# Kernel optimization log

Measured on AMD Instinct MI355X. Metric: run time of the kernel, lower is better.

Reference implementation:

```python
import jax, jax.numpy as jnp
import numpy as np

N = 100000      # num_nodes
E = 500000      # num_edges
D = 128         # memory_dim (also per-head out channels of TransformerConv)
EF = 16         # edge_feat_dim
H = 2           # heads
OUT = 64        # classifier out_channels


def setup_inputs() -> dict:
    key = jax.random.key(0)
    ks = jax.random.split(key, 24)
    g = lambda k, shape, s=0.05: (jax.random.normal(k, shape, jnp.float32) * s)
    inp = {
        "edge_index": jax.random.randint(ks[0], (2, E), 0, N, dtype=jnp.int64),
        "edge_attr": jax.random.normal(ks[1], (E, EF), jnp.float32),
        "edge_time": jax.random.uniform(ks[2], (E,), jnp.float32),
        # memory buffer (non-trainable in torch); randn so gathers are non-trivial
        "memory": g(ks[3], (N, D), 0.1),
        # MessageModule MLP: Linear(2D+EF -> D), ReLU, Linear(D -> D)
        "w1": g(ks[4], (2 * D + EF, D)), "b1": g(ks[5], (D,)),
        "w2": g(ks[6], (D, D)), "b2": g(ks[7], (D,)),
        # GRUCell(D, D): torch layout [3D, D] with gate order r,z,n
        "gru_wih": g(ks[8], (3 * D, D)), "gru_whh": g(ks[9], (3 * D, D)),
        "gru_bih": g(ks[10], (3 * D,)), "gru_bhh": g(ks[11], (3 * D,)),
        # TransformerConv(D, D, heads=H): lin_query/key/value: D -> H*D, lin_skip: D -> H*D
        "wq": g(ks[12], (D, H * D)), "bq": g(ks[13], (H * D,)),
        "wk": g(ks[14], (D, H * D)), "bk": g(ks[15], (H * D,)),
        "wv": g(ks[16], (D, H * D)), "bv": g(ks[17], (H * D,)),
        "wskip": g(ks[18], (D, H * D)), "bskip": g(ks[19], (H * D,)),
        # classifier: H*D -> OUT
        "wc": g(ks[20], (H * D, OUT)), "bc": g(ks[21], (OUT,)),
    }
    return inp


def reference(edge_index, edge_attr, edge_time, memory, w1, b1, w2, b2,
              gru_wih, gru_whh, gru_bih, gru_bhh,
              wq, bq, wk, bk, wv, bv, wskip, bskip, wc, bc):
    n_nodes = memory.shape[0]
    src, dst = edge_index[0], edge_index[1]
    # memory is a requires_grad=False parameter in torch
    mem = jax.lax.stop_gradient(memory)

    # ---- message computation (gather + MLP) ----
    src_mem = mem[src]                      # [E, D]
    dst_mem = mem[dst]                      # [E, D]
    msg_in = jnp.concatenate([src_mem, dst_mem, edge_attr], axis=-1)
    messages = jax.nn.relu(msg_in @ w1 + b1) @ w2 + b2   # [E, D]

    # ---- GRUCell memory update (torch gate order: r, z, n) ----
    gi = messages @ gru_wih.T + gru_bih     # [E, 3D]
    gh = dst_mem @ gru_whh.T + gru_bhh      # [E, 3D]
    i_r, i_z, i_n = jnp.split(gi, 3, axis=-1)
    h_r, h_z, h_n = jnp.split(gh, 3, axis=-1)
    r = jax.nn.sigmoid(i_r + h_r)
    z = jax.nn.sigmoid(i_z + h_z)
    n = jnp.tanh(i_n + r * h_n)
    new_mem = (1.0 - z) * n + z * dst_mem   # [E, D]
    # detached scatter write (memory.data[node_ids] = updated_mem.data)
    node_mem = mem.at[dst].set(jax.lax.stop_gradient(new_mem))  # [N, D]

    # ---- TransformerConv(D, D, heads=H), concat=True, root_weight=True ----
    q = (node_mem @ wq + bq).reshape(n_nodes, H, D)
    k = (node_mem @ wk + bk).reshape(n_nodes, H, D)
    v = (node_mem @ wv + bv).reshape(n_nodes, H, D)
    # per-edge attention logits, aggregated at destination node
    logits = jnp.sum(q[dst] * k[src], axis=-1) / jnp.sqrt(jnp.float32(D))  # [E, H]
    m = jax.ops.segment_max(logits, dst, num_segments=n_nodes)             # [N, H]
    ex = jnp.exp(logits - m[dst])
    s = jax.ops.segment_sum(ex, dst, num_segments=n_nodes)                 # [N, H]
    alpha = ex / (s[dst] + 1e-16)                                          # [E, H]
    agg = jax.ops.segment_sum(v[src] * alpha[..., None], dst,
                              num_segments=n_nodes)                        # [N, H, D]
    conv_out = agg.reshape(n_nodes, H * D) + node_mem @ wskip + bskip

    # ---- classifier ----
    return conv_out @ wc + bc               # [N, OUT]
```

## Files before the change

kernel.cpp:

```cpp
#include <hip/hip_runtime.h>
#include <hip/hip_bf16.h>

#define DD 128
#define EFD 16
#define HDIM 256
#define OUTD 64
#define AW 296

#define P_W1T 0
#define P_W2T 36864
#define P_WIH 53248
#define P_WHH 102400
#define P_QKV 151552
#define P_WSK 249856
#define P_WCT 282624
#define P_TOT 299008

using bf16 = __hip_bfloat16;
typedef __attribute__((ext_vector_type(8))) short fab;
typedef __attribute__((ext_vector_type(4))) float f4;

__device__ __forceinline__ float b2f(bf16 x){ return __bfloat162float(x); }
__device__ __forceinline__ bf16  f2b(float x){ return __float2bfloat16(x); }
__device__ __forceinline__ unsigned short us(bf16 x){ return *(unsigned short*)&x; }
__device__ __forceinline__ float rawbf(unsigned int u16){
  return __uint_as_float(u16 << 16);
}
__device__ __forceinline__ unsigned pk2(float a, float b){
  return (unsigned)us(f2b(a)) | ((unsigned)us(f2b(b)) << 16);
}
__device__ __forceinline__ float gw(const void* p, size_t i, int f32){
  return f32 ? ((const float*)p)[i] : b2f(((const bf16*)p)[i]);
}
__device__ __forceinline__ uint2 ld4bf(const void* base, size_t off, int f32){
  if(f32){
    float4 v = *(const float4*)((const float*)base + off);
    uint2 r;
    r.x = pk2(v.x, v.y);
    r.y = pk2(v.z, v.w);
    return r;
  }
  return *(const uint2*)((const bf16*)base + off);
}
__device__ __forceinline__ int geti(const int* ei, int is64, long long idx){
  return is64 ? ei[2*idx] : ei[(size_t)idx];
}
__device__ __forceinline__ int clampi(int x, int hi){
  return x < 0 ? 0 : (x >= hi ? hi-1 : x);
}

__global__ void k_detect(const int* __restrict__ ei,
                         const unsigned short* __restrict__ mem16,
                         int* __restrict__ flags){
  __shared__ int s64, sf32;
  int t = threadIdx.x;
  if(t == 0){ s64 = 1; sf32 = 0; }
  __syncthreads();
  if(ei[2*t + 1] != 0) atomicAnd(&s64, 0);
  int cnt = 0;
  for(int i = t; i < 4096; i += 256){
    unsigned short h = mem16[2*i];
    if((h & 0x7f80u) >= 0x4000u) cnt++;
  }
  atomicAdd(&sf32, cnt);
  __syncthreads();
  if(t == 0){ flags[0] = s64; flags[1] = (sf32 > 8) ? 1 : 0; }
}

__global__ void k_init(int* winner, int* cntrp, int N){
  int i = blockIdx.x*blockDim.x + threadIdx.x;
  if(i < N) winner[i] = -1;
  if(i <= N) cntrp[i] = 0;
}

__global__ void k_winner(const int* __restrict__ ei, const int* __restrict__ flags,
                         int* winner, int* cntrp, int E, int N){
  int e = blockIdx.x*blockDim.x + threadIdx.x;
  if(e >= E) return;
  int d = clampi(geti(ei, flags[0], (long long)E + e), N);
  atomicMax(&winner[d], e);
  atomicAdd(&cntrp[d], 1);
}

__global__ void k_scanA(const int* __restrict__ cnt, int* __restrict__ bsum, int N, int P){
  __shared__ int sd[256];
  int b = blockIdx.x, t = threadIdx.x;
  int base = (b*256 + t)*P;
  int s = 0;
  for(int p=0;p<P;p++){ int i = base+p; if(i<N) s += cnt[i]; }
  sd[t] = s; __syncthreads();
  for(int off=128; off>0; off>>=1){
    if(t<off) sd[t] += sd[t+off];
    __syncthreads();
  }
  if(t==0) bsum[b] = sd[0];
}

__global__ void k_scanB(const int* __restrict__ bsum, int* __restrict__ boff,
                        int* __restrict__ rowptr, int N, int E){
  __shared__ int sd[256];
  int t = threadIdx.x;
  int v = bsum[t];
  sd[t] = v; __syncthreads();
  for(int off=1; off<256; off<<=1){
    int u = (t>=off) ? sd[t-off] : 0;
    __syncthreads();
    sd[t] += u;
    __syncthreads();
  }
  boff[t] = sd[t] - v;
  if(t==0) rowptr[N] = E;
}

__global__ void k_scanC(int* __restrict__ cntrp, const int* __restrict__ boff,
                        int* __restrict__ head, int N, int P){
  __shared__ int sd[256];
  int b = blockIdx.x, t = threadIdx.x;
  int base = (b*256 + t)*P;
  int loc[8];
  int s = 0;
  for(int p=0;p<P;p++){ int i=base+p; int cc=(i<N)?cntrp[i]:0; loc[p]=s; s+=cc; }
  sd[t]=s; __syncthreads();
  for(int off=1; off<256; off<<=1){
    int u=(t>=off)?sd[t-off]:0;
    __syncthreads(); sd[t]+=u; __syncthreads();
  }
  int start = boff[b] + sd[t] - s;
  for(int p=0;p<P;p++){
    int i=base+p;
    if(i<N){ int r = start + loc[p]; cntrp[i]=r; head[i]=r; }
  }
}

__global__ void k_scatter(const int* __restrict__ ei, const int* __restrict__ flags,
                          int* __restrict__ head, int* __restrict__ esrc, int E, int N){
  int e = blockIdx.x*256 + threadIdx.x;
  if(e >= E) return;
  int is64 = flags[0];
  int src = clampi(geti(ei, is64, e), N);
  int dst = clampi(geti(ei, is64, (long long)E + e), N);
  int slot = atomicAdd(&head[dst], 1);
  esrc[slot] = src;
}

__global__ void k_pack(const void* w1, const void* w2, const void* wih, const void* whh,
                       const void* wq, const void* wk, const void* wv,
                       const void* wsk, const void* wc,
                       const int* __restrict__ flags, bf16* __restrict__ pk){
  int i = blockIdx.x*256 + threadIdx.x;
  if(i >= P_TOT) return;
  int f = flags[1];
  float v;
  if(i < P_W2T){ int j = i/288, c = i%288; v = (c < 272) ? gw(w1,(size_t)c*DD + j, f) : 0.f; }
  else if(i < P_WIH){ int r = i - P_W2T; int j = r>>7, c = r&127; v = gw(w2,(size_t)c*DD + j, f); }
  else if(i < P_WHH){ v = gw(wih, i - P_WIH, f); }
  else if(i < P_QKV){ v = gw(whh, i - P_WHH, f); }
  else if(i < P_WSK){
    int r = i - P_QKV; int jj = r>>7, c = r&127;
    int tb = jj>>8, j = jj&255;
    const void* w = (tb==0) ? wq : ((tb==1) ? wk : wv);
    v = gw(w, (size_t)c*HDIM + j, f);
  }
  else if(i < P_WCT){ int r = i - P_WSK; int j = r>>7, c = r&127; v = gw(wsk,(size_t)c*HDIM + j, f); }
  else { int r = i - P_WCT; int o = r>>8, j = r&255; v = gw(wc,(size_t)j*OUTD + o, f); }
  pk[i] = f2b(v);
}

__global__ __launch_bounds__(512) void k_msggru_qkv(
    const int* __restrict__ ei, const void* __restrict__ eattr,
    const void* __restrict__ mem, const bf16* __restrict__ pk,
    const void* b1, const void* b2, const void* bih, const void* bhh,
    const void* bq, const void* bk, const void* bv,
    const int* __restrict__ winner, const int* __restrict__ flags,
    bf16* __restrict__ node_mem, bf16* __restrict__ qt, bf16* __restrict__ kv, int N){
  const bf16* pw1T = pk + P_W1T;
  const bf16* pw2T = pk + P_W2T;
  const bf16* pwih = pk + P_WIH;
  const bf16* pwhh = pk + P_WHH;
  __shared__ bf16 Abuf[128][AW];
  __shared__ int swin[128], ssrc[128];
  int t = threadIdx.x;
  int n0 = blockIdx.x*128;
  int f = flags[1], is64 = flags[0];
  if(t < 128){
    int n = n0 + t;
    int w = (n < N) ? winner[n] : -1;
    swin[t] = w;
    ssrc[t] = (w >= 0) ? clampi(geti(ei, is64, w), N) : 0;
  }
  __syncthreads();
  const uint2 z2 = {0u, 0u};
  for(int idx=t; idx<128*32; idx+=512){
    int i = idx>>5, c4 = (idx&31)*4;
    int w = swin[i], n = n0+i;
    uint2 sv = (w>=0) ? ld4bf(mem, (size_t)ssrc[i]*DD + c4, f) : z2;
    uint2 dv = (n<N)  ? ld4bf(mem, (size_t)n*DD + c4, f)      : z2;
    *(uint2*)&Abuf[i][c4]    = sv;
    *(uint2*)&Abuf[i][DD+c4] = dv;
  }
  for(int idx=t; idx<128*4; idx+=512){
    int i = idx>>2, c4 = (idx&3)*4;
    uint2 v = (swin[i]>=0) ? ld4bf(eattr, (size_t)swin[i]*EFD + c4, f) : z2;
    *(uint2*)&Abuf[i][256+c4] = v;
  }
  for(int idx=t; idx<128*6; idx+=512){
    int i = idx/6, c4 = 272 + (idx%6)*4;
    *(uint2*)&Abuf[i][c4] = z2;
  }
  __syncthreads();

  int lane  = t & 63;
  int wid   = t >> 6;
  int col16 = lane & 15;
  int quad  = lane >> 4;
  int q8    = quad*8;
  int ch    = wid*16 + quad*4;

  {
    uint2 hres[8];
    const bf16* wrow = pw1T + (size_t)(wid*16 + col16)*288 + q8;
    fab w[9];
    #pragma unroll
    for(int kc=0;kc<9;kc++) w[kc] = *(const fab*)(wrow + kc*32);
    float bb0 = gw(b1, ch,   f), bb1 = gw(b1, ch+1, f);
    float bb2 = gw(b1, ch+2, f), bb3 = gw(b1, ch+3, f);
    #pragma unroll
    for(int mt=0; mt<8; mt++){
      f4 acc = (f4){0.f,0.f,0.f,0.f};
      #pragma unroll
      for(int kc=0;kc<9;kc++){
        fab an = *(const fab*)&Abuf[mt*16+col16][kc*32+q8];
        acc = __builtin_amdgcn_mfma_f32_16x16x32_bf16(w[kc], an, acc, 0,0,0);
      }
      uint2 hv;
      hv.x = pk2(fmaxf(acc[0]+bb0,0.f), fmaxf(acc[1]+bb1,0.f));
      hv.y = pk2(fmaxf(acc[2]+bb2,0.f), fmaxf(acc[3]+bb3,0.f));
      hres[mt] = hv;
    }
    __syncthreads();
    #pragma unroll
    for(int mt=0; mt<8; mt++)
      *(uint2*)&Abuf[mt*16+col16][ch] = hres[mt];
    __syncthreads();
  }

  {
    uint2 mres[8];
    const bf16* wrow = pw2T + (size_t)(wid*16 + col16)*128 + q8;
    fab w[4];
    #pragma unroll
    for(int kc=0;kc<4;kc++) w[kc] = *(const fab*)(wrow + kc*32);
    float bb0 = gw(b2, ch,   f), bb1 = gw(b2, ch+1, f);
    float bb2 = gw(b2, ch+2, f), bb3 = gw(b2, ch+3, f);
    #pragma unroll
    for(int mt=0; mt<8; mt++){
      f4 acc = (f4){0.f,0.f,0.f,0.f};
      #pragma unroll
      for(int kc=0;kc<4;kc++){
        fab an = *(const fab*)&Abuf[mt*16+col16][kc*32+q8];
        acc = __builtin_amdgcn_mfma_f32_16x16x32_bf16(w[kc], an, acc, 0,0,0);
      }
      uint2 hv;
      hv.x = pk2(acc[0]+bb0, acc[1]+bb1);
      hv.y = pk2(acc[2]+bb2, acc[3]+bb3);
      mres[mt] = hv;
    }
    __syncthreads();
    #pragma unroll
    for(int mt=0; mt<8; mt++)
      *(uint2*)&Abuf[mt*16+col16][ch] = mres[mt];
    __syncthreads();
  }

  {
    uint2 ovals[8];
    size_t row = (size_t)(wid*16 + col16)*128;
    const bf16* wi = pwih + row + q8;
    const bf16* wh = pwhh + row + q8;
    float bR0 = gw(bih,ch,f)+gw(bhh,ch,f),     bR1 = gw(bih,ch+1,f)+gw(bhh,ch+1,f);
    float bR2 = gw(bih,ch+2,f)+gw(bhh,ch+2,f), bR3 = gw(bih,ch+3,f)+gw(bhh,ch+3,f);
    float bZ0 = gw(bih,128+ch,f)+gw(bhh,128+ch,f), bZ1 = gw(bih,129+ch,f)+gw(bhh,129+ch,f);
    float bZ2 = gw(bih,130+ch,f)+gw(bhh,130+ch,f), bZ3 = gw(bih,131+ch,f)+gw(bhh,131+ch,f);
    float bNi0 = gw(bih,256+ch,f), bNi1 = gw(bih,257+ch,f);
    float bNi2 = gw(bih,258+ch,f), bNi3 = gw(bih,259+ch,f);
    float bNh0 = gw(bhh,256+ch,f), bNh1 = gw(bhh,257+ch,f);
    float bNh2 = gw(bhh,258+ch,f), bNh3 = gw(bhh,259+ch,f);
    #pragma unroll
    for(int mt=0; mt<8; mt++){
      int arow = mt*16 + col16;
      f4 ri=(f4){0,0,0,0}, zi=(f4){0,0,0,0}, ni=(f4){0,0,0,0};
      #pragma unroll
      for(int kc=0;kc<4;kc++){
        int kb = kc*32;
        fab am = *(const fab*)&Abuf[arow][kb+q8];
        ri = __builtin_amdgcn_mfma_f32_16x16x32_bf16(*(const fab*)(wi+kb),       am, ri, 0,0,0);
        zi = __builtin_amdgcn_mfma_f32_16x16x32_bf16(*(const fab*)(wi+16384+kb), am, zi, 0,0,0);
        ni = __builtin_amdgcn_mfma_f32_16x16x32_bf16(*(const fab*)(wi+32768+kb), am, ni, 0,0,0);
      }
      f4 rh=(f4){0,0,0,0}, zh=(f4){0,0,0,0}, nh=(f4){0,0,0,0};
      #pragma unroll
      for(int kc=0;kc<4;kc++){
        int kb = kc*32;
        fab ad = *(const fab*)&Abuf[arow][DD+kb+q8];
        rh = __builtin_amdgcn_mfma_f32_16x16x32_bf16(*(const fab*)(wh+kb),       ad, rh, 0,0,0);
        zh = __builtin_amdgcn_mfma_f32_16x16x32_bf16(*(const fab*)(wh+16384+kb), ad, zh, 0,0,0);
        nh = __builtin_amdgcn_mfma_f32_16x16x32_bf16(*(const fab*)(wh+32768+kb), ad, nh, 0,0,0);
      }
      bool upd = (swin[arow] >= 0);
      uint2 hraw = *(const uint2*)&Abuf[arow][DD+ch];
      float hp0 = rawbf(hraw.x & 0xffffu), hp1 = rawbf(hraw.x >> 16);
      float hp2 = rawbf(hraw.y & 0xffffu), hp3 = rawbf(hraw.y >> 16);
      float o0, o1, o2, o3;
      if(upd){
        float rr0 = 1.f/(1.f+__expf(-(ri[0]+rh[0]+bR0)));
        float rr1 = 1.f/(1.f+__expf(-(ri[1]+rh[1]+bR1)));
        float rr2 = 1.f/(1.f+__expf(-(ri[2]+rh[2]+bR2)));
        float rr3 = 1.f/(1.f+__expf(-(ri[3]+rh[3]+bR3)));
        float zz0 = 1.f/(1.f+__expf(-(zi[0]+zh[0]+bZ0)));
        float zz1 = 1.f/(1.f+__expf(-(zi[1]+zh[1]+bZ1)));
        float zz2 = 1.f/(1.f+__expf(-(zi[2]+zh[2]+bZ2)));
        float zz3 = 1.f/(1.f+__expf(-(zi[3]+zh[3]+bZ3)));
        float nn0 = tanhf(ni[0]+bNi0 + rr0*(nh[0]+bNh0));
        float nn1 = tanhf(ni[1]+bNi1 + rr1*(nh[1]+bNh1));
        float nn2 = tanhf(ni[2]+bNi2 + rr2*(nh[2]+bNh2));
        float nn3 = tanhf(ni[3]+bNi3 + rr3*(nh[3]+bNh3));
        o0 = (1.f-zz0)*nn0 + zz0*hp0;
        o1 = (1.f-zz1)*nn1 + zz1*hp1;
        o2 = (1.f-zz2)*nn2 + zz2*hp2;
        o3 = (1.f-zz3)*nn3 + zz3*hp3;
      } else { o0 = hp0; o1 = hp1; o2 = hp2; o3 = hp3; }
      uint2 ov;
      ov.x = pk2(o0, o1);
      ov.y = pk2(o2, o3);
      ovals[mt] = ov;
      int n = n0 + arow;
      if(n < N) *(uint2*)&node_mem[(size_t)n*DD + ch] = ov;
    }
    __syncthreads();
    #pragma unroll
    for(int mt=0; mt<8; mt++)
      *(uint2*)&Abuf[mt*16+col16][ch] = ovals[mt];
    __syncthreads();
  }

  {
    const bf16* pq = pk + P_QKV;
    #pragma unroll 2
    for(int i=0;i<6;i++){
      int nt = wid*6 + i;
      const bf16* wrow = pq + (size_t)(nt*16 + col16)*128 + q8;
      fab w[4];
      #pragma unroll
      for(int kc=0;kc<4;kc++) w[kc] = *(const fab*)(wrow + kc*32);
      int dch = nt*16 + quad*4;
      int tb = dch >> 8, j = dch & 255;
      const void* bp = (tb==0) ? bq : ((tb==1) ? bk : bv);
      float bb0 = gw(bp, j,   f), bb1 = gw(bp, j+1, f);
      float bb2 = gw(bp, j+2, f), bb3 = gw(bp, j+3, f);
      #pragma unroll
      for(int mt=0; mt<8; mt++){
        f4 acc = (f4){0.f,0.f,0.f,0.f};
        #pragma unroll
        for(int kc=0;kc<4;kc++){
          fab an = *(const fab*)&Abuf[mt*16+col16][kc*32+q8];
          acc = __builtin_amdgcn_mfma_f32_16x16x32_bf16(w[kc], an, acc, 0,0,0);
        }
        int n = n0 + mt*16 + col16;
        if(n < N){
          uint2 ov;
          ov.x = pk2(acc[0]+bb0, acc[1]+bb1);
          ov.y = pk2(acc[2]+bb2, acc[3]+bb3);
          if(tb==0) *(uint2*)&qt[(size_t)n*HDIM + j] = ov;
          else      *(uint2*)&kv[(size_t)n*512 + ((tb==1)?0:256) + j] = ov;
        }
      }
    }
  }
}

__global__ __launch_bounds__(256) void k_attn(
    const bf16* __restrict__ qt, const bf16* __restrict__ kv,
    const int* __restrict__ rowptr, const int* __restrict__ esrc,
    bf16* __restrict__ aggb, int N){
  int lane = threadIdx.x & 63;
  int n = blockIdx.x*4 + (threadIdx.x >> 6);
  if(n >= N) return;
  int beg = rowptr[n], end = rowptr[n+1];
  uint4 qa = *(const uint4*)(qt + (size_t)n*HDIM + 8*(lane & 31));
  float q0 = rawbf(qa.x & 0xffffu), q1 = rawbf(qa.x >> 16);
  float q2 = rawbf(qa.y & 0xffffu), q3 = rawbf(qa.y >> 16);
  float q4 = rawbf(qa.z & 0xffffu), q5 = rawbf(qa.z >> 16);
  float q6 = rawbf(qa.w & 0xffffu), q7 = rawbf(qa.w >> 16);
  float acc[8] = {0.f,0.f,0.f,0.f,0.f,0.f,0.f,0.f};
  float l = 0.f;
  for(int c = beg; c < end; c += 64){
    int se = (c + lane < end) ? esrc[c + lane] : 0;
    int ce = end - c; if(ce > 64) ce = 64;
    uint4 buf0 = {0u,0u,0u,0u}, buf1 = {0u,0u,0u,0u};
    int s0 = __shfl(se, 0, 64);
    buf0 = *(const uint4*)(kv + (size_t)s0*512 + 8*lane);
    if(ce > 1){
      int s1 = __shfl(se, 1, 64);
      buf1 = *(const uint4*)(kv + (size_t)s1*512 + 8*lane);
    }
    for(int j = 0; j < ce; j++){
      uint4 cur = buf0;
      buf0 = buf1;
      if(j + 2 < ce){
        int s2 = __shfl(se, j + 2, 64);
        buf1 = *(const uint4*)(kv + (size_t)s2*512 + 8*lane);
      }
      float p = q0*rawbf(cur.x & 0xffffu) + q1*rawbf(cur.x >> 16)
              + q2*rawbf(cur.y & 0xffffu) + q3*rawbf(cur.y >> 16)
              + q4*rawbf(cur.z & 0xffffu) + q5*rawbf(cur.z >> 16)
              + q6*rawbf(cur.w & 0xffffu) + q7*rawbf(cur.w >> 16);
      p += __shfl_xor(p, 8, 64); p += __shfl_xor(p, 4, 64);
      p += __shfl_xor(p, 2, 64); p += __shfl_xor(p, 1, 64);
      float ex = __expf(p * 0.08838834764831845f);
      l += ex;
      float exv = __shfl(ex, lane & 31, 64);
      acc[0] += exv*rawbf(cur.x & 0xffffu); acc[1] += exv*rawbf(cur.x >> 16);
      acc[2] += exv*rawbf(cur.y & 0xffffu); acc[3] += exv*rawbf(cur.y >> 16);
      acc[4] += exv*rawbf(cur.z & 0xffffu); acc[5] += exv*rawbf(cur.z >> 16);
      acc[6] += exv*rawbf(cur.w & 0xffffu); acc[7] += exv*rawbf(cur.w >> 16);
    }
  }
  float ls = __shfl(l, lane & 31, 64);
  if(lane >= 32){
    float li = 1.f/(ls + 1e-16f);
    uint4 w;
    w.x = pk2(acc[0]*li, acc[1]*li);
    w.y = pk2(acc[2]*li, acc[3]*li);
    w.z = pk2(acc[4]*li, acc[5]*li);
    w.w = pk2(acc[6]*li, acc[7]*li);
    *(uint4*)(aggb + (size_t)n*HDIM + 8*(lane - 32)) = w;
  }
}

__global__ __launch_bounds__(256) void k_cls_mfma(
    const bf16* __restrict__ node_mem, const bf16* __restrict__ aggb,
    const bf16* __restrict__ pk, const void* bsk, const void* bc,
    const int* __restrict__ flags, float* __restrict__ out, int N){
  __shared__ bf16 Abuf[64][128];
  __shared__ bf16 Cbuf[64][HDIM];
  int t = threadIdx.x, n0 = blockIdx.x*64, f = flags[1];
  for(int id=t; id<1024; id+=256){
    int i = id>>4, c8 = (id&15)*8;
    int n = n0 + i;
    uint4 val = {0u,0u,0u,0u};
    if(n < N) val = *(const uint4*)&node_mem[(size_t)n*DD + c8];
    *(uint4*)&Abuf[i][c8] = val;
  }
  __syncthreads();
  int lane = t&63, m0 = (t>>6)*16, col16 = lane&15, quad = lane>>4;
  {
    fab a[4];
    #pragma unroll
    for(int kc=0;kc<4;kc++) a[kc] = *(const fab*)&Abuf[m0+col16][kc*32+quad*8];
    const bf16* psk = pk + P_WSK;
    for(int nt=0;nt<16;nt++){
      f4 acc = (f4){0.f,0.f,0.f,0.f};
      #pragma unroll
      for(int kc=0;kc<4;kc++){
        fab b = *(const fab*)&psk[(size_t)(nt*16 + col16)*128 + kc*32+quad*8];
        acc = __builtin_amdgcn_mfma_f32_16x16x32_bf16(a[kc], b, acc, 0,0,0);
      }
      int j = nt*16 + col16;
      float bb = gw(bsk, j, f);
      #pragma unroll
      for(int r=0;r<4;r++){
        int row = m0 + quad*4 + r;
        int n = n0 + row;
        float cv = acc[r] + bb + ((n < N) ? b2f(aggb[(size_t)n*HDIM + j]) : 0.f);
        Cbuf[row][j] = f2b(cv);
      }
    }
  }
  __syncthreads();
  {
    fab a2[8];
    #pragma unroll
    for(int kc=0;kc<8;kc++) a2[kc] = *(const fab*)&Cbuf[m0+col16][kc*32+quad*8];
    const bf16* pct = pk + P_WCT;
    for(int nt=0;nt<4;nt++){
      f4 acc = (f4){0.f,0.f,0.f,0.f};
      #pragma unroll
      for(int kc=0;kc<8;kc++){
        fab b = *(const fab*)&pct[(size_t)(nt*16 + col16)*HDIM + kc*32+quad*8];
        acc = __builtin_amdgcn_mfma_f32_16x16x32_bf16(a2[kc], b, acc, 0,0,0);
      }
      int o = nt*16 + col16;
      float bb = gw(bc, o, f);
      #pragma unroll
      for(int r=0;r<4;r++){
        int n = n0 + m0 + quad*4 + r;
        if(n < N) out[(size_t)n*OUTD + o] = acc[r] + bb;
      }
    }
  }
}

extern "C" void kernel_launch(void* const* d_in, const int* in_sizes, int n_in,
                              void* d_out, int out_size, void* d_ws, size_t ws_size,
                              hipStream_t stream){
  const int*  ei    = (const int*)d_in[0];
  const void* eattr = d_in[1];
  const void* mem   = d_in[3];
  const void* w1  = d_in[4];  const void* b1  = d_in[5];
  const void* w2  = d_in[6];  const void* b2  = d_in[7];
  const void* wih = d_in[8];  const void* whh = d_in[9];
  const void* bih = d_in[10]; const void* bhh = d_in[11];
  const void* wq  = d_in[12]; const void* bq  = d_in[13];
  const void* wk  = d_in[14]; const void* bk  = d_in[15];
  const void* wv  = d_in[16]; const void* bv  = d_in[17];
  const void* wsk = d_in[18]; const void* bsk = d_in[19];
  const void* wc  = d_in[20]; const void* bc  = d_in[21];
  float* out = (float*)d_out;
  const int E = in_sizes[2];
  const int N = in_sizes[3] / DD;

  char* p = (char*)d_ws;
  auto alloc = [&](size_t bytes)->char*{
    char* r = p; p += (bytes + 511) & ~(size_t)511; return r;
  };
  int*   flags  = (int*)  alloc(8);
  int*   winner = (int*)  alloc((size_t)N*4);
  bf16*  pk     = (bf16*) alloc((size_t)P_TOT*2);
  bf16*  node_mem = (bf16*)alloc((size_t)N*DD*2);
  bf16*  kv   = (bf16*)alloc((size_t)N*512*2);
  bf16*  qt   = (bf16*)alloc((size_t)N*HDIM*2);
  bf16*  aggb = qt;
  int*   cntrp = (int*)alloc(((size_t)N+1)*4);
  int*   head  = (int*)alloc((size_t)N*4);
  int*   bsum  = (int*)alloc(256*4);
  int*   boff  = (int*)alloc(256*4);
  int*   esrc  = (int*)alloc((size_t)E*4);

  size_t required = (size_t)(p - (char*)d_ws);
  if(required > ws_size) return;

  const int P = (N + 256*256 - 1) / (256*256);

  hipLaunchKernelGGL(k_detect, dim3(1), dim3(256), 0, stream,
                     ei, (const unsigned short*)mem, flags);
  hipLaunchKernelGGL(k_init,   dim3((N+256)/256), dim3(256), 0, stream, winner, cntrp, N);
  hipLaunchKernelGGL(k_winner, dim3((E+255)/256), dim3(256), 0, stream,
                     ei, flags, winner, cntrp, E, N);
  hipLaunchKernelGGL(k_pack,   dim3((P_TOT+255)/256), dim3(256), 0, stream,
                     w1, w2, wih, whh, wq, wk, wv, wsk, wc, flags, pk);
  hipLaunchKernelGGL(k_msggru_qkv, dim3((N+127)/128), dim3(512), 0, stream,
                     ei, eattr, mem, pk, b1, b2, bih, bhh, bq, bk, bv,
                     winner, flags, node_mem, qt, kv, N);
  hipLaunchKernelGGL(k_scanA, dim3(256), dim3(256), 0, stream, cntrp, bsum, N, P);
  hipLaunchKernelGGL(k_scanB, dim3(1),   dim3(256), 0, stream, bsum, boff, cntrp, N, E);
  hipLaunchKernelGGL(k_scanC, dim3(256), dim3(256), 0, stream, cntrp, boff, head, N, P);
  hipLaunchKernelGGL(k_scatter, dim3((E+255)/256), dim3(256), 0, stream,
                     ei, flags, head, esrc, E, N);
  hipLaunchKernelGGL(k_attn, dim3((N+3)/4), dim3(256), 0, stream,
                     qt, kv, cntrp, esrc, aggb, N);
  hipLaunchKernelGGL(k_cls_mfma, dim3((N+63)/64), dim3(256), 0, stream,
                     node_mem, aggb, pk, bsk, bc, flags, out, N);
}
```

Before: 662.4 us.

## Restructure classifier MFMA to transpose operands, pad LDS, vectorize epilogue stores

```diff
diff --git a/kernel.cpp b/kernel.cpp
--- a/kernel.cpp
+++ b/kernel.cpp
@@ -441,8 +441,8 @@
     const bf16* __restrict__ node_mem, const bf16* __restrict__ aggb,
     const bf16* __restrict__ pk, const void* bsk, const void* bc,
     const int* __restrict__ flags, float* __restrict__ out, int N){
-  __shared__ bf16 Abuf[64][128];
-  __shared__ bf16 Cbuf[64][HDIM];
+  __shared__ bf16 Abuf[64][136];
+  __shared__ bf16 Cbuf[64][264];
   int t = threadIdx.x, n0 = blockIdx.x*64, f = flags[1];
   for(int id=t; id<1024; id+=256){
     int i = id>>4, c8 = (id&15)*8;
@@ -452,49 +452,59 @@
     *(uint4*)&Abuf[i][c8] = val;
   }
   __syncthreads();
-  int lane = t&63, m0 = (t>>6)*16, col16 = lane&15, quad = lane>>4;
+  int lane = t&63, wid = t>>6, col16 = lane&15, quad = lane>>4, q8 = quad*8;
   {
-    fab a[4];
-    #pragma unroll
-    for(int kc=0;kc<4;kc++) a[kc] = *(const fab*)&Abuf[m0+col16][kc*32+quad*8];
     const bf16* psk = pk + P_WSK;
-    for(int nt=0;nt<16;nt++){
-      f4 acc = (f4){0.f,0.f,0.f,0.f};
-      #pragma unroll
-      for(int kc=0;kc<4;kc++){
-        fab b = *(const fab*)&psk[(size_t)(nt*16 + col16)*128 + kc*32+quad*8];
-        acc = __builtin_amdgcn_mfma_f32_16x16x32_bf16(a[kc], b, acc, 0,0,0);
-      }
-      int j = nt*16 + col16;
-      float bb = gw(bsk, j, f);
-      #pragma unroll
-      for(int r=0;r<4;r++){
-        int row = m0 + quad*4 + r;
-        int n = n0 + row;
-        float cv = acc[r] + bb + ((n < N) ? b2f(aggb[(size_t)n*HDIM + j]) : 0.f);
-        Cbuf[row][j] = f2b(cv);
+    #pragma unroll
+    for(int i=0;i<4;i++){
+      int nt = wid*4 + i;
+      const bf16* wrow = psk + (size_t)(nt*16 + col16)*128 + q8;
+      fab w[4];
+      #pragma unroll
+      for(int kc=0;kc<4;kc++) w[kc] = *(const fab*)(wrow + kc*32);
+      int ch = nt*16 + quad*4;
+      float bb0 = gw(bsk, ch,   f), bb1 = gw(bsk, ch+1, f);
+      float bb2 = gw(bsk, ch+2, f), bb3 = gw(bsk, ch+3, f);
+      #pragma unroll
+      for(int mt=0; mt<4; mt++){
+        f4 acc = (f4){0.f,0.f,0.f,0.f};
+        #pragma unroll
+        for(int kc=0;kc<4;kc++){
+          fab an = *(const fab*)&Abuf[mt*16+col16][kc*32+q8];
+          acc = __builtin_amdgcn_mfma_f32_16x16x32_bf16(w[kc], an, acc, 0,0,0);
+        }
+        int n = n0 + mt*16 + col16;
+        uint2 ag = {0u,0u};
+        if(n < N) ag = *(const uint2*)&aggb[(size_t)n*HDIM + ch];
+        uint2 cv;
+        cv.x = pk2(acc[0]+bb0+rawbf(ag.x & 0xffffu), acc[1]+bb1+rawbf(ag.x >> 16));
+        cv.y = pk2(acc[2]+bb2+rawbf(ag.y & 0xffffu), acc[3]+bb3+rawbf(ag.y >> 16));
+        *(uint2*)&Cbuf[mt*16+col16][ch] = cv;
       }
     }
   }
   __syncthreads();
   {
-    fab a2[8];
-    #pragma unroll
-    for(int kc=0;kc<8;kc++) a2[kc] = *(const fab*)&Cbuf[m0+col16][kc*32+quad*8];
     const bf16* pct = pk + P_WCT;
-    for(int nt=0;nt<4;nt++){
+    const bf16* wrow = pct + (size_t)(wid*16 + col16)*HDIM + q8;
+    fab w2[8];
+    #pragma unroll
+    for(int kc=0;kc<8;kc++) w2[kc] = *(const fab*)(wrow + kc*32);
+    int och = wid*16 + quad*4;
+    float bb0 = gw(bc, och,   f), bb1 = gw(bc, och+1, f);
+    float bb2 = gw(bc, och+2, f), bb3 = gw(bc, och+3, f);
+    #pragma unroll
+    for(int mt=0; mt<4; mt++){
       f4 acc = (f4){0.f,0.f,0.f,0.f};
       #pragma unroll
       for(int kc=0;kc<8;kc++){
-        fab b = *(const fab*)&pct[(size_t)(nt*16 + col16)*HDIM + kc*32+quad*8];
-        acc = __builtin_amdgcn_mfma_f32_16x16x32_bf16(a2[kc], b, acc, 0,0,0);
-      }
-      int o = nt*16 + col16;
-      float bb = gw(bc, o, f);
-      #pragma unroll
-      for(int r=0;r<4;r++){
-        int n = n0 + m0 + quad*4 + r;
-        if(n < N) out[(size_t)n*OUTD + o] = acc[r] + bb;
+        fab a2 = *(const fab*)&Cbuf[mt*16+col16][kc*32+q8];
+        acc = __builtin_amdgcn_mfma_f32_16x16x32_bf16(w2[kc], a2, acc, 0,0,0);
+      }
+      int n = n0 + mt*16 + col16;
+      if(n < N){
+        float4 ov = {acc[0]+bb0, acc[1]+bb1, acc[2]+bb2, acc[3]+bb3};
+        *(float4*)&out[(size_t)n*OUTD + och] = ov;
       }
     }
   }
```

After: 599.0 us. 1.11x faster.
